# Kernel tuning notes

Hardware: AMD Instinct MI355X
Metric: run time of the kernel (lower is better)

The kernel has to match this reference:

```python
import jax, jax.numpy as jnp
import numpy as np

N = 50000   # nodes
E = 800000  # edges
R = 8       # relations
B = 4       # bases
NEG = 0.2   # leaky relu slope


def setup_inputs() -> dict:
    key = jax.random.key(0)
    ks = jax.random.split(key, 20)
    s = 0.1
    rn = lambda k, sh: jax.random.normal(k, sh, dtype=jnp.float32) * s
    return {
        "x": jax.random.normal(ks[0], (N, 64), dtype=jnp.float32),
        "edge_index": jax.random.randint(ks[1], (2, E), 0, N),
        "edge_type": jax.random.randint(ks[2], (E,), 0, R),
        # RGCN layer 1 (64 -> 64), basis decomposition
        "basis1": rn(ks[3], (B, 64, 64)), "comp1": rn(ks[4], (R, B)),
        "root1": rn(ks[5], (64, 64)), "brg1": jnp.zeros((64,), jnp.float32),
        # GAT layer 1 (64 -> 32, heads=4, concat -> 128)
        "wg1": rn(ks[6], (64, 128)), "asrc1": rn(ks[7], (4, 32)),
        "adst1": rn(ks[8], (4, 32)), "bg1": jnp.zeros((128,), jnp.float32),
        # RGCN layer 2 (128 -> 32)
        "basis2": rn(ks[9], (B, 128, 32)), "comp2": rn(ks[10], (R, B)),
        "root2": rn(ks[11], (128, 32)), "brg2": jnp.zeros((32,), jnp.float32),
        # GAT layer 2 (32 -> 16, heads=4, concat=False -> mean)
        "wg2": rn(ks[12], (32, 64)), "asrc2": rn(ks[13], (4, 16)),
        "adst2": rn(ks[14], (4, 16)), "bg2": jnp.zeros((16,), jnp.float32),
    }


def rgcn(x, src, dst, etype, basis, comp, root, bias):
    """PyG RGCNConv with basis decomposition, aggr='mean' per relation."""
    n, f = x.shape
    weight = jnp.einsum('rb,bio->rio', comp, basis)          # [R, in, out]
    seg = dst * R + etype                                    # per (node, relation) segment
    msg = x[src]                                             # [E, in] gather
    sums = jax.ops.segment_sum(msg, seg, num_segments=n * R).reshape(n, R, f)
    cnt = jax.ops.segment_sum(jnp.ones((src.shape[0],), x.dtype), seg,
                              num_segments=n * R).reshape(n, R, 1)
    mean = sums / jnp.maximum(cnt, 1.0)                      # [N, R, in]
    return jnp.einsum('nri,rio->no', mean, weight) + x @ root + bias


def gat(x, src, dst, w, a_src, a_dst, bias, heads, out_ch, concat):
    """PyG GATConv: add self loops, edge softmax over incoming edges."""
    n = x.shape[0]
    loop = jnp.arange(n)
    s2 = jnp.concatenate([src, loop])
    d2 = jnp.concatenate([dst, loop])
    h = (x @ w).reshape(n, heads, out_ch)                    # [N, H, C]
    al_src = (h * a_src).sum(-1)                             # [N, H]
    al_dst = (h * a_dst).sum(-1)                             # [N, H]
    e = jax.nn.leaky_relu(al_src[s2] + al_dst[d2], NEG)      # [E2, H]
    m = jax.ops.segment_max(e, d2, num_segments=n)           # stable softmax per dst
    e = jnp.exp(e - m[d2])
    z = jax.ops.segment_sum(e, d2, num_segments=n)
    alpha = e / z[d2]                                        # [E2, H]
    msg = h[s2] * alpha[:, :, None]                          # [E2, H, C]
    out = jax.ops.segment_sum(msg, d2, num_segments=n)       # [N, H, C]
    out = out.reshape(n, heads * out_ch) if concat else out.mean(axis=1)
    return out + bias


def reference(x, edge_index, edge_type,
              basis1, comp1, root1, brg1, wg1, asrc1, adst1, bg1,
              basis2, comp2, root2, brg2, wg2, asrc2, adst2, bg2):
    src, dst = edge_index[0], edge_index[1]
    # i=0: RGCN + relu (dropout p=0)
    x = jax.nn.relu(rgcn(x, src, dst, edge_type, basis1, comp1, root1, brg1))
    # i=1 == 2*pairs-1: GAT concat, NO activation
    x = gat(x, src, dst, wg1, asrc1, adst1, bg1, heads=4, out_ch=32, concat=True)
    # i=2: RGCN + relu
    x = jax.nn.relu(rgcn(x, src, dst, edge_type, basis2, comp2, root2, brg2))
    # i=3: GAT mean-heads + relu
    x = jax.nn.relu(gat(x, src, dst, wg2, asrc2, adst2, bg2, heads=4, out_ch=16, concat=False))
    return jnp.tanh(x)
```

## Files before the change

kernel.cpp:

```cpp
#include <hip/hip_runtime.h>
#include <math.h>

#define NN 50000
#define EE 800000
#define RR 8
#define SLOPE 0.2f
#define SEGS (NN * RR)
#define NTW ((NN + 63) / 64)
#define NBUK 98
#define SEGB 4096
#define EB4 ((EE + 4095) / 4096)

typedef __attribute__((ext_vector_type(8))) short bf16x8;
typedef __attribute__((ext_vector_type(4))) float f32x4;
typedef _Float16 f16;
typedef __attribute__((ext_vector_type(4))) _Float16 h4;
typedef __attribute__((ext_vector_type(8))) _Float16 h8;

__device__ __forceinline__ float leaky(float v) { return v >= 0.f ? v : SLOPE * v; }

__device__ __forceinline__ void fmacc(float4& a, const float4& v, float p) {
    a.x = fmaf(v.x, p, a.x);
    a.y = fmaf(v.y, p, a.y);
    a.z = fmaf(v.z, p, a.z);
    a.w = fmaf(v.w, p, a.w);
}

__device__ __forceinline__ void red4(float4& a, int m) {
    a.x += __shfl_xor(a.x, m);
    a.y += __shfl_xor(a.y, m);
    a.z += __shfl_xor(a.z, m);
    a.w += __shfl_xor(a.w, m);
}

__device__ __forceinline__ float4 h4tof4(h4 t) {
    return make_float4((float)t[0], (float)t[1], (float)t[2], (float)t[3]);
}

__device__ __forceinline__ h4 hmax4(h4 a, h4 b) {
    h4 r;
    r[0] = a[0] > b[0] ? a[0] : b[0];
    r[1] = a[1] > b[1] ? a[1] : b[1];
    r[2] = a[2] > b[2] ? a[2] : b[2];
    r[3] = a[3] > b[3] ? a[3] : b[3];
    return r;
}

__device__ __forceinline__ void split8(const float4& v0, const float4& v1,
                                       bf16x8& hi, bf16x8& lo) {
    float e[8] = {v0.x, v0.y, v0.z, v0.w, v1.x, v1.y, v1.z, v1.w};
    union { bf16x8 v; unsigned u[4]; } H, L;
#pragma unroll
    for (int j = 0; j < 4; j++) {
        unsigned b0 = __float_as_uint(e[2 * j]), b1 = __float_as_uint(e[2 * j + 1]);
        unsigned h0 = b0 & 0xFFFF0000u, h1 = b1 & 0xFFFF0000u;
        H.u[j] = (h0 >> 16) | h1;
        float l0 = e[2 * j] - __uint_as_float(h0);
        float l1 = e[2 * j + 1] - __uint_as_float(h1);
        L.u[j] = (__float_as_uint(l0) >> 16) | (__float_as_uint(l1) & 0xFFFF0000u);
    }
    hi = H.v;
    lo = L.v;
}

__global__ __launch_bounds__(256) void k_hist(const int* __restrict__ dst,
                                              int* __restrict__ buccnt) {
    __shared__ int h[NBUK];
    int tid = threadIdx.x;
    for (int i = tid; i < NBUK; i += 256) h[i] = 0;
    __syncthreads();
    int e0 = blockIdx.x * 4096;
    int cnt = EE - e0;
    if (cnt > 4096) cnt = 4096;
    for (int i = tid; i < cnt; i += 256) atomicAdd(&h[dst[e0 + i] >> 9], 1);
    __syncthreads();
    for (int i = tid; i < NBUK; i += 256)
        if (h[i]) atomicAdd(&buccnt[i], h[i]);
}

__global__ void k_scan98(const int* __restrict__ buccnt, int* __restrict__ bucbase,
                         int* __restrict__ cbcur) {
    __shared__ int sh[128];
    int t = threadIdx.x;
    int v = (t < NBUK) ? buccnt[t] : 0;
    sh[t] = v;
    __syncthreads();
    for (int off = 1; off < 128; off <<= 1) {
        int u = (t >= off) ? sh[t - off] : 0;
        __syncthreads();
        sh[t] += u;
        __syncthreads();
    }
    int excl = sh[t] - v;
    if (t <= NBUK) bucbase[t] = excl;
    if (t < NBUK) cbcur[t] = excl;
}

__global__ __launch_bounds__(256) void k_fillA(const int* __restrict__ src,
                                               const int* __restrict__ dst,
                                               const int* __restrict__ et,
                                               int* __restrict__ cbcur,
                                               int* __restrict__ recbuf) {
    __shared__ int hist[NBUK], lcur[NBUK], gres[NBUK];
    int tid = threadIdx.x;
    int e0 = blockIdx.x * 4096;
    int cnt = EE - e0;
    if (cnt > 4096) cnt = 4096;
    for (int i = tid; i < NBUK; i += 256) { hist[i] = 0; lcur[i] = 0; }
    __syncthreads();
    int myb[16], myrec[16];
#pragma unroll
    for (int j = 0; j < 16; j++) {
        int i = tid + j * 256;
        if (i < cnt) {
            int e = e0 + i;
            int d = dst[e];
            int b = d >> 9;
            myb[j] = b;
            myrec[j] = ((d & 511) << 19) | (src[e] << 3) | et[e];
            atomicAdd(&hist[b], 1);
        } else {
            myb[j] = -1;
            myrec[j] = 0;
        }
    }
    __syncthreads();
    if (tid < NBUK) gres[tid] = atomicAdd(&cbcur[tid], hist[tid]);
    __syncthreads();
#pragma unroll
    for (int j = 0; j < 16; j++) {
        if (myb[j] >= 0) {
            int p = atomicAdd(&lcur[myb[j]], 1);
            recbuf[gres[myb[j]] + p] = myrec[j];
        }
    }
}

__global__ __launch_bounds__(256) void k_fillB2(const int* __restrict__ bucbase,
                                                const int* __restrict__ recbuf,
                                                int* __restrict__ rp,
                                                int* __restrict__ srcs2) {
    __shared__ int cnt[SEGB];
    __shared__ int psc[256];
    int b = blockIdx.x;
    int segbase = b * SEGB;
    int nseg = SEGS - segbase;
    if (nseg > SEGB) nseg = SEGB;
    int base = bucbase[b];
    int cntE = bucbase[b + 1] - base;
    int tid = threadIdx.x;
    for (int s = tid; s < SEGB; s += 256) cnt[s] = 0;
    __syncthreads();
    for (int i = tid; i < cntE; i += 256) {
        int rec = recbuf[base + i];
        int segl = ((rec >> 19) << 3) | (rec & 7);
        atomicAdd(&cnt[segl], 1);
    }
    __syncthreads();
    int loc[16];
    int sbase = tid * 16;
    int run = 0;
#pragma unroll
    for (int j = 0; j < 16; j++) { loc[j] = cnt[sbase + j]; run += loc[j]; }
    psc[tid] = run;
    __syncthreads();
    for (int off = 1; off < 256; off <<= 1) {
        int u = (tid >= off) ? psc[tid - off] : 0;
        __syncthreads();
        psc[tid] += u;
        __syncthreads();
    }
    int excl = psc[tid] - run;
#pragma unroll
    for (int j = 0; j < 16; j++) {
        int s = sbase + j;
        int v = loc[j];
        cnt[s] = excl;
        if (s < nseg) rp[segbase + s] = base + excl;
        excl += v;
    }
    __syncthreads();
    for (int i = tid; i < cntE; i += 256) {
        int rec = recbuf[base + i];
        int segl = ((rec >> 19) << 3) | (rec & 7);
        int p = atomicAdd(&cnt[segl], 1);
        srcs2[base + p] = rec & 0x7FFFF;
    }
    if (b == NBUK - 1 && tid == 0) rp[SEGS] = EE;
}

__global__ void k_xh(const float* __restrict__ X, f16* __restrict__ xh) {
    int i = blockIdx.x * 256 + threadIdx.x;
    if (i >= NN * 8) return;
    float4 v0 = *(const float4*)(X + (size_t)i * 8);
    float4 v1 = *(const float4*)(X + (size_t)i * 8 + 4);
    h8 hv = {(f16)v0.x, (f16)v0.y, (f16)v0.z, (f16)v0.w,
             (f16)v1.x, (f16)v1.y, (f16)v1.z, (f16)v1.w};
    *(h8*)(xh + (size_t)i * 8) = hv;
}

__global__ void k_prep(const float* __restrict__ wg1, const float* __restrict__ wg2,
                       const float* __restrict__ root1, const float* __restrict__ root2,
                       const float* __restrict__ basis1, const float* __restrict__ basis2,
                       const float* __restrict__ comp2,
                       const float* __restrict__ asrc1, const float* __restrict__ adst1,
                       const float* __restrict__ asrc2, const float* __restrict__ adst2,
                       float* __restrict__ Wcat2e, float* __restrict__ wg1r,
                       float* __restrict__ Wstk, float* __restrict__ U1p,
                       float* __restrict__ U2p, float* __restrict__ Wb1) {
    int idx = blockIdx.x * 256 + threadIdx.x;
    if (idx < 16384) {
        int h = idx >> 12, kc = idx & 4095;
        int k = kc >> 6, c = kc & 63;
        wg1r[idx] = (c < 32) ? wg1[k * 128 + h * 32 + c] : 0.f;
    } else if (idx < 24576) {
        int j = idx - 16384;
        int row = j >> 6, c = j & 63;
        int h = row >> 5, k = row & 31;
        Wstk[j] = (c < 16) ? wg2[k * 64 + h * 16 + c] : 0.f;
    } else if (idx < 32768) {
        int j = idx - 24576;
        int k = j >> 6, c = j & 63;
        Wcat2e[k * 320 + c] = (c < 32) ? root2[k * 32 + c] : 0.f;
    } else if (idx < 36864) {
        int j0 = idx - 32768;
        int k = j0 >> 6, j = j0 & 63;
        float s = 0.f;
        if (j < 8) {
            int h = j & 3;
            const float* a = (j < 4) ? asrc1 : adst1;
            for (int c = 0; c < 32; c++) s += wg1[k * 128 + h * 32 + c] * a[h * 32 + c];
        }
        U1p[j0] = s;
    } else if (idx < 38912) {
        int j0 = idx - 36864;
        int k = j0 >> 6, j = j0 & 63;
        float s = 0.f;
        if (j < 8) {
            int h = j & 3;
            const float* a = (j < 4) ? asrc2 : adst2;
            for (int c = 0; c < 16; c++) s += wg2[k * 64 + h * 16 + c] * a[h * 16 + c];
        }
        U2p[j0] = s;
    } else if (idx < 55296) {
        Wb1[idx - 38912] = basis1[idx - 38912];
    } else if (idx < 59392) {
        Wb1[idx - 38912] = root1[idx - 55296];
    } else if (idx < 92160) {
        int j = idx - 59392;
        int i = j >> 8, rc = j & 255;
        int r = rc >> 5, o = rc & 31;
        float acc = 0.f;
#pragma unroll
        for (int b = 0; b < 4; b++) acc += comp2[r * 4 + b] * basis2[b * 4096 + i * 32 + o];
        Wcat2e[i * 320 + 64 + rc] = acc;
    }
}

__global__ void k_pack(const float* __restrict__ Wb1, const float* __restrict__ wg1r,
                       const float* __restrict__ Wcat, short* __restrict__ pWb1,
                       short* __restrict__ pwg1r, short* __restrict__ pWcat) {
    int u = blockIdx.x * 256 + threadIdx.x;
    int lane = u & 63, pair = u >> 6;
    if (pair >= 136) return;
    int m = lane & 15, g = lane >> 4;
    const float* src;
    int ldB, col, k0;
    short* dst;
    if (pair < 40) {
        int ct = pair / 10, kc = pair % 10;
        src = Wb1; ldB = 64; col = ct * 16 + m; k0 = kc * 32 + g * 8;
        dst = pWb1 + pair * 1024 + lane * 8;
    } else if (pair < 56) {
        int q = pair - 40;
        int h = q >> 2, lp = q & 3, ct = lp >> 1, kc = lp & 1;
        src = wg1r + h * 4096; ldB = 64; col = ct * 16 + m; k0 = kc * 32 + g * 8;
        dst = pwg1r + q * 1024 + lane * 8;
    } else {
        int q = pair - 56;
        int p = q >> 4, lp = q & 15, ct = lp >> 2, kc = lp & 3;
        src = Wcat; ldB = 320; col = p * 64 + ct * 16 + m; k0 = kc * 32 + g * 8;
        dst = pWcat + q * 1024 + lane * 8;
    }
    float e[8];
#pragma unroll
    for (int r = 0; r < 8; r++) e[r] = src[(size_t)(k0 + r) * ldB + col];
    union { bf16x8 v; unsigned u4[4]; } H, L;
#pragma unroll
    for (int j = 0; j < 4; j++) {
        unsigned b0 = __float_as_uint(e[2 * j]), b1 = __float_as_uint(e[2 * j + 1]);
        unsigned h0 = b0 & 0xFFFF0000u, h1 = b1 & 0xFFFF0000u;
        H.u4[j] = (h0 >> 16) | h1;
        float l0 = e[2 * j] - __uint_as_float(h0);
        float l1 = e[2 * j + 1] - __uint_as_float(h1);
        L.u4[j] = (__float_as_uint(l0) >> 16) | (__float_as_uint(l1) & 0xFFFF0000u);
    }
    *(bf16x8*)dst = H.v;
    *(bf16x8*)(dst + 512) = L.v;
}

template <int KTOT, int NCOL, int ACT = 0, int OUTH = 0, int AH = 0>
__global__ __launch_bounds__(256) void k_mfma(const float* __restrict__ X, int ldX, int xmb,
                                              const short* __restrict__ Bpk, int bmb,
                                              float* __restrict__ Y, int ldY, size_t ymb,
                                              const float* __restrict__ bias, int biasmb) {
    constexpr int NKC = KTOT / 32;
    constexpr int NCT = NCOL / 16;
    const int tid = threadIdx.x;
    const int wid = tid >> 6, lane = tid & 63;
    const int m = lane & 15, g = lane >> 4;
    const int mb = blockIdx.y;
    const int rowbase = blockIdx.x * 64 + wid * 16;
    if (rowbase >= NN) return;
    const float* Xm = X + (size_t)mb * xmb + (size_t)(rowbase + m) * ldX;
    const f16* Xmh = (const f16*)X + (size_t)mb * xmb + (size_t)(rowbase + m) * ldX;
    const short* Bm = Bpk + (size_t)mb * bmb;

    f32x4 acc[NCT];
#pragma unroll
    for (int c = 0; c < NCT; c++) acc[c] = (f32x4){0.f, 0.f, 0.f, 0.f};

#pragma unroll
    for (int kc = 0; kc < NKC; kc++) {
        float4 v0, v1;
        if (AH) {
            h8 hv = *(const h8*)(Xmh + kc * 32 + g * 8);
            v0 = make_float4((float)hv[0], (float)hv[1], (float)hv[2], (float)hv[3]);
            v1 = make_float4((float)hv[4], (float)hv[5], (float)hv[6], (float)hv[7]);
        } else {
            v0 = *(const float4*)(Xm + kc * 32 + g * 8);
            v1 = *(const float4*)(Xm + kc * 32 + g * 8 + 4);
        }
        bf16x8 ah, al;
        split8(v0, v1, ah, al);
#pragma unroll
        for (int ct = 0; ct < NCT; ct++) {
            const short* bp = Bm + (size_t)(ct * NKC + kc) * 1024 + lane * 8;
            bf16x8 bh = *(const bf16x8*)bp;
            bf16x8 bl = *(const bf16x8*)(bp + 512);
            acc[ct] = __builtin_amdgcn_mfma_f32_16x16x32_bf16(ah, bh, acc[ct], 0, 0, 0);
            acc[ct] = __builtin_amdgcn_mfma_f32_16x16x32_bf16(al, bh, acc[ct], 0, 0, 0);
            acc[ct] = __builtin_amdgcn_mfma_f32_16x16x32_bf16(ah, bl, acc[ct], 0, 0, 0);
        }
    }

#pragma unroll
    for (int ct = 0; ct < NCT; ct++) {
        int col = ct * 16 + m;
        float bv = bias ? bias[mb * biasmb + col] : 0.f;
#pragma unroll
        for (int i = 0; i < 4; i++) {
            float o = acc[ct][i] + bv;
            if (ACT == 2) o = fmaxf(o, 0.f);
            if (OUTH) {
                f16* Yh = (f16*)Y;
                Yh[(size_t)mb * ymb + (size_t)(rowbase + g * 4 + i) * ldY + col] = (f16)o;
            } else {
                Y[(size_t)mb * ymb + (size_t)(rowbase + g * 4 + i) * ldY + col] = o;
            }
        }
    }
}

__global__ __launch_bounds__(256) void k_mfmaL3(const f16* __restrict__ Xh,
                                                const short* __restrict__ Bpk,
                                                float* __restrict__ x3,
                                                f16* __restrict__ ybuf3h) {
    const int tid = threadIdx.x;
    const int wid = tid >> 6, lane = tid & 63;
    const int m = lane & 15, g = lane >> 4;
    const int y = blockIdx.y;
    const int rowbase = blockIdx.x * 64 + wid * 16;
    if (rowbase >= NN) return;
    const f16* Xm = Xh + (size_t)(rowbase + m) * 128;

    f32x4 acc[6];
#pragma unroll
    for (int j = 0; j < 6; j++) acc[j] = (f32x4){0.f, 0.f, 0.f, 0.f};

#pragma unroll
    for (int kc = 0; kc < 4; kc++) {
        h8 hv = *(const h8*)(Xm + kc * 32 + g * 8);
        float4 v0 = make_float4((float)hv[0], (float)hv[1], (float)hv[2], (float)hv[3]);
        float4 v1 = make_float4((float)hv[4], (float)hv[5], (float)hv[6], (float)hv[7]);
        bf16x8 ah, al;
        split8(v0, v1, ah, al);
#pragma unroll
        for (int j = 0; j < 6; j++) {
            int bct = (y == 0) ? ((j < 2) ? j : j + 2) : (8 + (y - 1) * 6 + j);
            const short* bp = Bpk + (size_t)(bct * 4 + kc) * 1024 + lane * 8;
            bf16x8 bh = *(const bf16x8*)bp;
            bf16x8 bl = *(const bf16x8*)(bp + 512);
            acc[j] = __builtin_amdgcn_mfma_f32_16x16x32_bf16(ah, bh, acc[j], 0, 0, 0);
            acc[j] = __builtin_amdgcn_mfma_f32_16x16x32_bf16(al, bh, acc[j], 0, 0, 0);
            acc[j] = __builtin_amdgcn_mfma_f32_16x16x32_bf16(ah, bl, acc[j], 0, 0, 0);
        }
    }
#pragma unroll
    for (int j = 0; j < 6; j++) {
        int bct = (y == 0) ? ((j < 2) ? j : j + 2) : (8 + (y - 1) * 6 + j);
        if (bct < 2) {
            int col = bct * 16 + m;
#pragma unroll
            for (int r = 0; r < 4; r++) {
                int n = rowbase + g * 4 + r;
                x3[(size_t)n * 32 + col] = acc[j][r];
            }
        } else {
            int gcol = bct * 16 + m - 64;
            int p = gcol >> 6, cc = gcol & 63;
            f16* Yp = ybuf3h + (size_t)p * NN * 64;
#pragma unroll
            for (int r = 0; r < 4; r++) {
                int n = rowbase + g * 4 + r;
                Yp[(size_t)n * 64 + cc] = (f16)acc[j][r];
            }
        }
    }
}

__global__ __launch_bounds__(256) void k_gagg1(const int* __restrict__ rp,
                                               const int* __restrict__ srcs2,
                                               const float* __restrict__ comp,
                                               const f16* __restrict__ Xh,
                                               f16* __restrict__ Uh) {
    __shared__ float4 sh_w[4][8];
    int wid = threadIdx.x >> 6, lane = threadIdx.x & 63;
    int n = blockIdx.x * 4 + wid;
    int rpv = (lane <= 8) ? rp[n * RR + lane] : 0;
    int nxt = __shfl(rpv, (lane + 1) & 63);
    if (lane < 8) {
        float inv = 1.f / (float)((nxt - rpv) > 0 ? (nxt - rpv) : 1);
        float4 c = *(const float4*)(comp + lane * 4);
        sh_w[wid][lane] = make_float4(c.x * inv, c.y * inv, c.z * inv, c.w * inv);
    }
    int q = lane & 15;
    int beg = rp[n * RR], end = rp[n * RR + RR];
    float4 a0 = make_float4(0.f, 0.f, 0.f, 0.f);
    float4 a1 = a0, a2 = a0, a3 = a0;
    int k = beg + (lane >> 4);
    for (; k + 4 < end; k += 8) {
        int key0 = srcs2[k], key1 = srcs2[k + 4];
        float4 w0 = sh_w[wid][key0 & 7], w1 = sh_w[wid][key1 & 7];
        float4 v0 = h4tof4(*(const h4*)(Xh + (size_t)(key0 >> 3) * 64 + q * 4));
        float4 v1 = h4tof4(*(const h4*)(Xh + (size_t)(key1 >> 3) * 64 + q * 4));
        fmacc(a0, v0, w0.x);
        fmacc(a1, v0, w0.y);
        fmacc(a2, v0, w0.z);
        fmacc(a3, v0, w0.w);
        fmacc(a0, v1, w1.x);
        fmacc(a1, v1, w1.y);
        fmacc(a2, v1, w1.z);
        fmacc(a3, v1, w1.w);
    }
    if (k < end) {
        int key0 = srcs2[k];
        float4 w0 = sh_w[wid][key0 & 7];
        float4 v0 = h4tof4(*(const h4*)(Xh + (size_t)(key0 >> 3) * 64 + q * 4));
        fmacc(a0, v0, w0.x);
        fmacc(a1, v0, w0.y);
        fmacc(a2, v0, w0.z);
        fmacc(a3, v0, w0.w);
    }
    red4(a0, 16); red4(a0, 32);
    red4(a1, 16); red4(a1, 32);
    red4(a2, 16); red4(a2, 32);
    red4(a3, 16); red4(a3, 32);
    if (lane < 16) {
        f16* un = Uh + (size_t)n * 320;
        h4 o0 = {(f16)a0.x, (f16)a0.y, (f16)a0.z, (f16)a0.w};
        h4 o1 = {(f16)a1.x, (f16)a1.y, (f16)a1.z, (f16)a1.w};
        h4 o2 = {(f16)a2.x, (f16)a2.y, (f16)a2.z, (f16)a2.w};
        h4 o3 = {(f16)a3.x, (f16)a3.y, (f16)a3.z, (f16)a3.w};
        *(h4*)(un + 0 * 64 + q * 4) = o0;
        *(h4*)(un + 1 * 64 + q * 4) = o1;
        *(h4*)(un + 2 * 64 + q * 4) = o2;
        *(h4*)(un + 3 * 64 + q * 4) = o3;
        *(h4*)(un + 256 + q * 4) = *(const h4*)(Xh + (size_t)n * 64 + q * 4);
    }
}

__global__ __launch_bounds__(256) void k_alds1(const f16* __restrict__ X1h,
                                               const float* __restrict__ U1p,
                                               f16* __restrict__ aldsEh) {
    __shared__ float sUT[8 * 68];
    int tid = threadIdx.x;
    for (int i = tid; i < 512; i += 256) {
        int j = i >> 6, c = i & 63;
        sUT[j * 68 + c] = U1p[c * 64 + j];
    }
    __syncthreads();
    int lane = tid & 63, wid = tid >> 6;
    int n = blockIdx.x * 32 + wid * 8 + (lane >> 3);
    int q = lane & 7;
    float x[8];
    if (n < NN) {
        h8 hv = *(const h8*)(X1h + (size_t)n * 64 + q * 8);
#pragma unroll
        for (int c = 0; c < 8; c++) x[c] = (float)hv[c];
    } else {
#pragma unroll
        for (int c = 0; c < 8; c++) x[c] = 0.f;
    }
    float al[8];
#pragma unroll
    for (int j = 0; j < 8; j++) {
        const float* u = &sUT[j * 68 + q * 8];
        float s = 0.f;
#pragma unroll
        for (int c = 0; c < 8; c++) s += x[c] * u[c];
        al[j] = s;
    }
#pragma unroll
    for (int m = 1; m < 8; m <<= 1)
#pragma unroll
        for (int j = 0; j < 8; j++) al[j] += __shfl_xor(al[j], m);
    if (n < NN) {
        float av = al[q];
        int pos = (q < 4) ? q : q + 4;
        aldsEh[(size_t)n * 16 + pos] = (f16)__expf(av);
        aldsEh[(size_t)n * 16 + pos + 4] = (f16)__expf(SLOPE * av);
    }
}

__global__ __launch_bounds__(256) void k_final(const f16* __restrict__ Xm,
                                               const float* __restrict__ Wstk,
                                               const float* __restrict__ bg2,
                                               float* __restrict__ out) {
    __shared__ float sWT[16 * 132];
    int tid = threadIdx.x;
    for (int i = tid; i < 2048; i += 256) {
        int c = i >> 7, k = i & 127;
        sWT[c * 132 + k] = Wstk[k * 64 + c];
    }
    __syncthreads();
    int lane = tid & 63, wid = tid >> 6;
    int n = blockIdx.x * 32 + wid * 8 + (lane >> 3);
    int q = lane & 7;
    float x[16];
    if (n < NN) {
#pragma unroll
        for (int t = 0; t < 4; t++) {
            float4 v = h4tof4(*(const h4*)(Xm + (size_t)n * 128 + t * 32 + q * 4));
            x[t * 4 + 0] = v.x; x[t * 4 + 1] = v.y; x[t * 4 + 2] = v.z; x[t * 4 + 3] = v.w;
        }
    } else {
#pragma unroll
        for (int k = 0; k < 16; k++) x[k] = 0.f;
    }
    float al[16];
#pragma unroll
    for (int c = 0; c < 16; c++) {
        float s = 0.f;
#pragma unroll
        for (int t = 0; t < 4; t++) {
            const float* w = &sWT[c * 132 + t * 32 + q * 4];
            s += x[t * 4 + 0] * w[0] + x[t * 4 + 1] * w[1] + x[t * 4 + 2] * w[2] +
                 x[t * 4 + 3] * w[3];
        }
        al[c] = s;
    }
#pragma unroll
    for (int m = 1; m < 8; m <<= 1)
#pragma unroll
        for (int c = 0; c < 16; c++) al[c] += __shfl_xor(al[c], m);
    if (n < NN && q < 4) {
        float4 bv = *(const float4*)(bg2 + q * 4);
        float4 v;
        v.x = tanhf(fmaxf(0.25f * al[q * 4 + 0] + bv.x, 0.f));
        v.y = tanhf(fmaxf(0.25f * al[q * 4 + 1] + bv.y, 0.f));
        v.z = tanhf(fmaxf(0.25f * al[q * 4 + 2] + bv.z, 0.f));
        v.w = tanhf(fmaxf(0.25f * al[q * 4 + 3] + bv.w, 0.f));
        *(float4*)(out + (size_t)n * 16 + q * 4) = v;
    }
}

__global__ __launch_bounds__(256) void k_agg2(const int* __restrict__ rp,
                                              const int* __restrict__ srcs2,
                                              const f16* __restrict__ y,
                                              const float* __restrict__ bias,
                                              const float* __restrict__ U2p,
                                              const float* __restrict__ x3prev,
                                              f16* __restrict__ x3h,
                                              f16* __restrict__ aldsEh) {
    __shared__ float sh_inv[4][8];
    int wid = threadIdx.x >> 6, lane = threadIdx.x & 63;
    int n = blockIdx.x * 4 + wid;
    int rpv = (lane <= 8) ? rp[n * RR + lane] : 0;
    int nxt = __shfl(rpv, (lane + 1) & 63);
    if (lane < 8) sh_inv[wid][lane] = 1.f / (float)((nxt - rpv) > 0 ? (nxt - rpv) : 1);
    int q = lane & 7;
    int beg = rp[n * RR], end = rp[n * RR + RR];
    float4 acc = make_float4(0.f, 0.f, 0.f, 0.f);
    int k = beg + (lane >> 3);
    for (; k + 8 < end; k += 16) {
        int key0 = srcs2[k], key1 = srcs2[k + 8];
        int s0 = key0 >> 3, s1 = key1 >> 3;
        int g0 = key0 & 7, g1 = key1 & 7;
        float e0 = sh_inv[wid][g0], e1 = sh_inv[wid][g1];
        float4 v0 = h4tof4(*(const h4*)(y + ((size_t)(g0 >> 1) * NN + s0) * 64 + (g0 & 1) * 32 + q * 4));
        float4 v1 = h4tof4(*(const h4*)(y + ((size_t)(g1 >> 1) * NN + s1) * 64 + (g1 & 1) * 32 + q * 4));
        fmacc(acc, v0, e0);
        fmacc(acc, v1, e1);
    }
    if (k < end) {
        int key0 = srcs2[k];
        int s0 = key0 >> 3;
        int g0 = key0 & 7;
        float4 v0 = h4tof4(*(const h4*)(y + ((size_t)(g0 >> 1) * NN + s0) * 64 + (g0 & 1) * 32 + q * 4));
        fmacc(acc, v0, sh_inv[wid][g0]);
    }
    red4(acc, 8);
    red4(acc, 16);
    red4(acc, 32);
    if (lane < 8) {
        float4 prev = *(const float4*)(x3prev + (size_t)n * 32 + q * 4);
        float4 b = *(const float4*)(bias + q * 4);
        float4 v;
        v.x = fmaxf(prev.x + acc.x + b.x, 0.f);
        v.y = fmaxf(prev.y + acc.y + b.y, 0.f);
        v.z = fmaxf(prev.z + acc.z + b.z, 0.f);
        v.w = fmaxf(prev.w + acc.w + b.w, 0.f);
        h4 hv = {(f16)v.x, (f16)v.y, (f16)v.z, (f16)v.w};
        *(h4*)(x3h + (size_t)n * 32 + q * 4) = hv;
        float al[8];
#pragma unroll
        for (int j = 0; j < 8; j++) {
            al[j] = fmaf(v.x, U2p[(q * 4 + 0) * 64 + j],
                    fmaf(v.y, U2p[(q * 4 + 1) * 64 + j],
                    fmaf(v.z, U2p[(q * 4 + 2) * 64 + j],
                         v.w * U2p[(q * 4 + 3) * 64 + j])));
        }
#pragma unroll
        for (int m = 1; m < 8; m <<= 1) {
#pragma unroll
            for (int j = 0; j < 8; j++) al[j] += __shfl_xor(al[j], m);
        }
        float av = al[q];
        int pos = (q < 4) ? q : q + 4;
        aldsEh[(size_t)n * 16 + pos] = (f16)__expf(av);
        aldsEh[(size_t)n * 16 + pos + 4] = (f16)__expf(SLOPE * av);
    }
}

template <int F, int LDX = F>
__global__ __launch_bounds__(256) void k_gatx(const int* __restrict__ rp,
                                              const int* __restrict__ srcs2,
                                              const f16* __restrict__ aldsEh,
                                              const f16* __restrict__ X,
                                              f16* __restrict__ msg) {
    constexpr int G = F / 4;
    constexpr int NG = 64 / G;
    int wid = threadIdx.x >> 6, lane = threadIdx.x & 63;
    int n = blockIdx.x * 4 + wid;
    if (n >= NN) return;
    int g = lane / G, q = lane % G;
    h4 EdH = *(const h4*)(aldsEh + (size_t)n * 16 + 8);
    h4 Ed2H = *(const h4*)(aldsEh + (size_t)n * 16 + 12);
    float4 acc0 = make_float4(0.f, 0.f, 0.f, 0.f);
    float4 acc1 = acc0, acc2 = acc0, acc3 = acc0;
    float4 z = make_float4(0.f, 0.f, 0.f, 0.f);
    if (g == 0) {
        h4 es = *(const h4*)(aldsEh + (size_t)n * 16);
        h4 es2 = *(const h4*)(aldsEh + (size_t)n * 16 + 4);
        float4 xv = h4tof4(*(const h4*)(X + (size_t)n * LDX + q * 4));
        h4 pH = hmax4(es * EdH, es2 * Ed2H);
        float p0 = (float)pH[0], p1 = (float)pH[1], p2 = (float)pH[2], p3 = (float)pH[3];
        z = make_float4(p0, p1, p2, p3);
        fmacc(acc0, xv, p0);
        fmacc(acc1, xv, p1);
        fmacc(acc2, xv, p2);
        fmacc(acc3, xv, p3);
    }
    int beg = rp[n * RR], end = rp[n * RR + RR];
    int k = beg + g;
    for (; k + NG < end; k += 2 * NG) {
        int s0 = srcs2[k] >> 3, s1 = srcs2[k + NG] >> 3;
        h8 e0 = *(const h8*)(aldsEh + (size_t)s0 * 16);
        h8 e1 = *(const h8*)(aldsEh + (size_t)s1 * 16);
        float4 x0 = h4tof4(*(const h4*)(X + (size_t)s0 * LDX + q * 4));
        float4 x1v = h4tof4(*(const h4*)(X + (size_t)s1 * LDX + q * 4));
        h4 e0lo = {e0[0], e0[1], e0[2], e0[3]};
        h4 e0hi = {e0[4], e0[5], e0[6], e0[7]};
        h4 e1lo = {e1[0], e1[1], e1[2], e1[3]};
        h4 e1hi = {e1[4], e1[5], e1[6], e1[7]};
        h4 p0H = hmax4(e0lo * EdH, e0hi * Ed2H);
        h4 p1H = hmax4(e1lo * EdH, e1hi * Ed2H);
        float p00 = (float)p0H[0], p01 = (float)p0H[1], p02 = (float)p0H[2], p03 = (float)p0H[3];
        float p10 = (float)p1H[0], p11 = (float)p1H[1], p12 = (float)p1H[2], p13 = (float)p1H[3];
        z.x += p00 + p10;
        z.y += p01 + p11;
        z.z += p02 + p12;
        z.w += p03 + p13;
        fmacc(acc0, x0, p00);
        fmacc(acc1, x0, p01);
        fmacc(acc2, x0, p02);
        fmacc(acc3, x0, p03);
        fmacc(acc0, x1v, p10);
        fmacc(acc1, x1v, p11);
        fmacc(acc2, x1v, p12);
        fmacc(acc3, x1v, p13);
    }
    if (k < end) {
        int s0 = srcs2[k] >> 3;
        h8 e0 = *(const h8*)(aldsEh + (size_t)s0 * 16);
        float4 x0 = h4tof4(*(const h4*)(X + (size_t)s0 * LDX + q * 4));
        h4 e0lo = {e0[0], e0[1], e0[2], e0[3]};
        h4 e0hi = {e0[4], e0[5], e0[6], e0[7]};
        h4 p0H = hmax4(e0lo * EdH, e0hi * Ed2H);
        float p00 = (float)p0H[0], p01 = (float)p0H[1], p02 = (float)p0H[2], p03 = (float)p0H[3];
        z.x += p00;
        z.y += p01;
        z.z += p02;
        z.w += p03;
        fmacc(acc0, x0, p00);
        fmacc(acc1, x0, p01);
        fmacc(acc2, x0, p02);
        fmacc(acc3, x0, p03);
    }
#pragma unroll
    for (int m = G; m < 64; m <<= 1) {
        red4(acc0, m);
        red4(acc1, m);
        red4(acc2, m);
        red4(acc3, m);
        red4(z, m);
    }
    if (g == 0) {
        float4 iz = make_float4(1.f / z.x, 1.f / z.y, 1.f / z.z, 1.f / z.w);
        f16* mp = msg + (size_t)n * 4 * F + q * 4;
        h4 o0 = {(f16)(acc0.x * iz.x), (f16)(acc0.y * iz.x), (f16)(acc0.z * iz.x), (f16)(acc0.w * iz.x)};
        h4 o1 = {(f16)(acc1.x * iz.y), (f16)(acc1.y * iz.y), (f16)(acc1.z * iz.y), (f16)(acc1.w * iz.y)};
        h4 o2 = {(f16)(acc2.x * iz.z), (f16)(acc2.y * iz.z), (f16)(acc2.z * iz.z), (f16)(acc2.w * iz.z)};
        h4 o3 = {(f16)(acc3.x * iz.w), (f16)(acc3.y * iz.w), (f16)(acc3.z * iz.w), (f16)(acc3.w * iz.w)};
        *(h4*)(mp + 0 * F) = o0;
        *(h4*)(mp + 1 * F) = o1;
        *(h4*)(mp + 2 * F) = o2;
        *(h4*)(mp + 3 * F) = o3;
    }
}

extern "C" void kernel_launch(void* const* d_in, const int* in_sizes, int n_in,
                              void* d_out, int out_size, void* d_ws, size_t ws_size,
                              hipStream_t stream) {
    const float* x      = (const float*)d_in[0];
    const int*   ei     = (const int*)d_in[1];
    const int*   et     = (const int*)d_in[2];
    const float* basis1 = (const float*)d_in[3];
    const float* comp1  = (const float*)d_in[4];
    const float* root1  = (const float*)d_in[5];
    const float* brg1   = (const float*)d_in[6];
    const float* wg1    = (const float*)d_in[7];
    const float* asrc1  = (const float*)d_in[8];
    const float* adst1  = (const float*)d_in[9];
    const float* bg1    = (const float*)d_in[10];
    const float* basis2 = (const float*)d_in[11];
    const float* comp2  = (const float*)d_in[12];
    const float* root2  = (const float*)d_in[13];
    const float* brg2   = (const float*)d_in[14];
    const float* wg2    = (const float*)d_in[15];
    const float* asrc2  = (const float*)d_in[16];
    const float* adst2  = (const float*)d_in[17];
    const float* bg2    = (const float*)d_in[18];
    const int* src = ei;
    const int* dst = ei + EE;
    float* out = (float*)d_out;

    int* wsi = (int*)d_ws;
    size_t ioff = 0;
    auto ialloc = [&](size_t n) { int* p = wsi + ioff; ioff += (n + 3) & ~(size_t)3; return p; };
    int* rp   = ialloc(SEGS + 1);
    int* srcs2 = ialloc(EE);
    int* recbuf = ialloc(EE);
    int* cbcur = ialloc(128);
    int* buccnt = ialloc(128);
    int* bucbase = ialloc(128);
    float* wsf = (float*)(wsi + ioff);
    size_t total_f = (ws_size - ioff * sizeof(int)) / sizeof(float);
    size_t P_f = (size_t)NN * 320;
    size_t need_f = P_f + (size_t)NN * 128
                  + 40960 + 20480 + 16384 + 8192 + 4096 + 2048
                  + (size_t)NN * 8
                  + 20480 + 8192 + 40960
                  + (size_t)NN * 32 + (size_t)NN * 16 + (size_t)NN * 32 + 64;
    if (total_f < need_f) return;
    size_t foff = 0;
    auto falloc = [&](size_t n) { float* p = wsf + foff; foff += (n + 3) & ~(size_t)3; return p; };
    float* P      = falloc(P_f);
    float* x2     = falloc((size_t)NN * 128);
    float* Wcat2e = falloc(40960);
    float* Wb1    = falloc(20480);
    float* wg1r   = falloc(16384);
    float* Wstk   = falloc(8192);
    float* U1p    = falloc(4096);
    float* U2p    = falloc(2048);
    f16* aldsEh   = (f16*)falloc((size_t)NN * 8);
    short* Wb1pk  = (short*)falloc(20480);
    short* wg1rpk = (short*)falloc(8192);
    short* Wcatpk = (short*)falloc(40960);
    f16* x1h      = (f16*)falloc((size_t)NN * 32);
    f16* x3h      = (f16*)falloc((size_t)NN * 16);
    f16* xh       = (f16*)falloc((size_t)NN * 32);
    f16* Uh = (f16*)P;
    f16* x2h = (f16*)x2;
    f16* msg1h  = (f16*)P;
    float* x3   = P;
    f16* ybuf3h = (f16*)(P + (size_t)NN * 64);
    f16* msg2h  = (f16*)(P + (size_t)NN * 64);

    const int NB4 = (NN + 3) / 4;
    const int NB32 = (NN + 31) / 32;

    hipMemsetAsync(buccnt, 0, 128 * sizeof(int), stream);
    k_hist<<<EB4, 256, 0, stream>>>(dst, buccnt);
    k_scan98<<<1, 128, 0, stream>>>(buccnt, bucbase, cbcur);
    k_fillA<<<EB4, 256, 0, stream>>>(src, dst, et, cbcur, recbuf);
    k_fillB2<<<NBUK, 256, 0, stream>>>(bucbase, recbuf, rp, srcs2);
    k_xh<<<(NN * 8 + 255) / 256, 256, 0, stream>>>(x, xh);
    k_prep<<<(92160 + 255) / 256, 256, 0, stream>>>(
        wg1, wg2, root1, root2, basis1, basis2, comp2, asrc1, adst1, asrc2, adst2,
        Wcat2e, wg1r, Wstk, U1p, U2p, Wb1);
    k_pack<<<34, 256, 0, stream>>>(Wb1, wg1r, Wcat2e, Wb1pk, wg1rpk, Wcatpk);

    k_gagg1<<<NB4, 256, 0, stream>>>(rp, srcs2, comp1, xh, Uh);
    k_mfma<320, 64, 2, 1, 1><<<dim3(NTW, 1), 256, 0, stream>>>((const float*)Uh, 320, 0,
                                                               Wb1pk, 0,
                                                               (float*)x1h, 64, 0, brg1, 0);

    k_alds1<<<NB32, 256, 0, stream>>>(x1h, U1p, aldsEh);
    k_gatx<64, 64><<<NB4, 256, 0, stream>>>(rp, srcs2, aldsEh, x1h, msg1h);
    k_mfma<64, 32, 0, 1, 1><<<dim3(NTW, 4), 256, 0, stream>>>((const float*)msg1h, 256, 64,
                                                              wg1rpk, 4096,
                                                              (float*)x2h, 128, 32, bg1, 32);

    k_mfmaL3<<<dim3(NTW, 3), 256, 0, stream>>>(x2h, Wcatpk, x3, ybuf3h);
    k_agg2<<<NB4, 256, 0, stream>>>(rp, srcs2, ybuf3h, brg2, U2p, x3, x3h, aldsEh);

    k_gatx<32, 32><<<NB4, 256, 0, stream>>>(rp, srcs2, aldsEh, x3h, msg2h);
    k_final<<<NB32, 256, 0, stream>>>(msg2h, Wstk, bg2, out);
}
```

Baseline: 386.9 us.

## Switch to fp16 MFMA and fp16 accumulation; fuse histogram with x conversion

Replaces the 3-pass bf16 hi/lo split MFMA with a 2-pass fp16 scheme (fp16 activations times hi/lo fp16 weights). The gather-aggregation kernels (gagg1, gatx) now accumulate in packed fp16 instead of fp32. Separately, the x-to-fp16 conversion kernel is merged into the edge histogram kernel to save a launch. This cuts MFMA count, conversion ALU work and register pressure, at the risk of fp16 overflow or precision loss in long accumulations over high-degree nodes.

```diff
diff --git a/kernel.cpp b/kernel.cpp
--- a/kernel.cpp
+++ b/kernel.cpp
@@ -10,14 +10,12 @@
 #define NBUK 98
 #define SEGB 4096
 #define EB4 ((EE + 4095) / 4096)
-
-typedef __attribute__((ext_vector_type(8))) short bf16x8;
+#define XB ((NN * 8 + 255) / 256)
+
 typedef __attribute__((ext_vector_type(4))) float f32x4;
 typedef _Float16 f16;
 typedef __attribute__((ext_vector_type(4))) _Float16 h4;
 typedef __attribute__((ext_vector_type(8))) _Float16 h8;
-
-__device__ __forceinline__ float leaky(float v) { return v >= 0.f ? v : SLOPE * v; }
 
 __device__ __forceinline__ void fmacc(float4& a, const float4& v, float p) {
     a.x = fmaf(v.x, p, a.x);
@@ -46,36 +44,34 @@
     return r;
 }
 
-__device__ __forceinline__ void split8(const float4& v0, const float4& v1,
-                                       bf16x8& hi, bf16x8& lo) {
-    float e[8] = {v0.x, v0.y, v0.z, v0.w, v1.x, v1.y, v1.z, v1.w};
-    union { bf16x8 v; unsigned u[4]; } H, L;
-#pragma unroll
-    for (int j = 0; j < 4; j++) {
-        unsigned b0 = __float_as_uint(e[2 * j]), b1 = __float_as_uint(e[2 * j + 1]);
-        unsigned h0 = b0 & 0xFFFF0000u, h1 = b1 & 0xFFFF0000u;
-        H.u[j] = (h0 >> 16) | h1;
-        float l0 = e[2 * j] - __uint_as_float(h0);
-        float l1 = e[2 * j + 1] - __uint_as_float(h1);
-        L.u[j] = (__float_as_uint(l0) >> 16) | (__float_as_uint(l1) & 0xFFFF0000u);
-    }
-    hi = H.v;
-    lo = L.v;
-}
-
-__global__ __launch_bounds__(256) void k_hist(const int* __restrict__ dst,
-                                              int* __restrict__ buccnt) {
+__device__ __forceinline__ h4 hsplat(f16 s) { return (h4){s, s, s, s}; }
+
+__global__ __launch_bounds__(256) void k_histxh(const int* __restrict__ dst,
+                                                int* __restrict__ buccnt,
+                                                const float* __restrict__ X,
+                                                f16* __restrict__ xh) {
     __shared__ int h[NBUK];
+    int b = blockIdx.x;
     int tid = threadIdx.x;
-    for (int i = tid; i < NBUK; i += 256) h[i] = 0;
-    __syncthreads();
-    int e0 = blockIdx.x * 4096;
-    int cnt = EE - e0;
-    if (cnt > 4096) cnt = 4096;
-    for (int i = tid; i < cnt; i += 256) atomicAdd(&h[dst[e0 + i] >> 9], 1);
-    __syncthreads();
-    for (int i = tid; i < NBUK; i += 256)
-        if (h[i]) atomicAdd(&buccnt[i], h[i]);
+    if (b < EB4) {
+        for (int i = tid; i < NBUK; i += 256) h[i] = 0;
+        __syncthreads();
+        int e0 = b * 4096;
+        int cnt = EE - e0;
+        if (cnt > 4096) cnt = 4096;
+        for (int i = tid; i < cnt; i += 256) atomicAdd(&h[dst[e0 + i] >> 9], 1);
+        __syncthreads();
+        for (int i = tid; i < NBUK; i += 256)
+            if (h[i]) atomicAdd(&buccnt[i], h[i]);
+    } else {
+        int i = (b - EB4) * 256 + tid;
+        if (i >= NN * 8) return;
+        float4 v0 = *(const float4*)(X + (size_t)i * 8);
+        float4 v1 = *(const float4*)(X + (size_t)i * 8 + 4);
+        h8 hv = {(f16)v0.x, (f16)v0.y, (f16)v0.z, (f16)v0.w,
+                 (f16)v1.x, (f16)v1.y, (f16)v1.z, (f16)v1.w};
+        *(h8*)(xh + (size_t)i * 8) = hv;
+    }
 }
 
 __global__ void k_scan98(const int* __restrict__ buccnt, int* __restrict__ bucbase,
@@ -187,16 +183,6 @@
         srcs2[base + p] = rec & 0x7FFFF;
     }
     if (b == NBUK - 1 && tid == 0) rp[SEGS] = EE;
-}
-
-__global__ void k_xh(const float* __restrict__ X, f16* __restrict__ xh) {
-    int i = blockIdx.x * 256 + threadIdx.x;
-    if (i >= NN * 8) return;
-    float4 v0 = *(const float4*)(X + (size_t)i * 8);
-    float4 v1 = *(const float4*)(X + (size_t)i * 8 + 4);
-    h8 hv = {(f16)v0.x, (f16)v0.y, (f16)v0.z, (f16)v0.w,
-             (f16)v1.x, (f16)v1.y, (f16)v1.z, (f16)v1.w};
-    *(h8*)(xh + (size_t)i * 8) = hv;
 }
 
 __global__ void k_prep(const float* __restrict__ wg1, const float* __restrict__ wg2,
@@ -282,25 +268,20 @@
         src = Wcat; ldB = 320; col = p * 64 + ct * 16 + m; k0 = kc * 32 + g * 8;
         dst = pWcat + q * 1024 + lane * 8;
     }
-    float e[8];
-#pragma unroll
-    for (int r = 0; r < 8; r++) e[r] = src[(size_t)(k0 + r) * ldB + col];
-    union { bf16x8 v; unsigned u4[4]; } H, L;
-#pragma unroll
-    for (int j = 0; j < 4; j++) {
-        unsigned b0 = __float_as_uint(e[2 * j]), b1 = __float_as_uint(e[2 * j + 1]);
-        unsigned h0 = b0 & 0xFFFF0000u, h1 = b1 & 0xFFFF0000u;
-        H.u4[j] = (h0 >> 16) | h1;
-        float l0 = e[2 * j] - __uint_as_float(h0);
-        float l1 = e[2 * j + 1] - __uint_as_float(h1);
-        L.u4[j] = (__float_as_uint(l0) >> 16) | (__float_as_uint(l1) & 0xFFFF0000u);
-    }
-    *(bf16x8*)dst = H.v;
-    *(bf16x8*)(dst + 512) = L.v;
-}
-
-template <int KTOT, int NCOL, int ACT = 0, int OUTH = 0, int AH = 0>
-__global__ __launch_bounds__(256) void k_mfma(const float* __restrict__ X, int ldX, int xmb,
+    h8 H, L;
+#pragma unroll
+    for (int r = 0; r < 8; r++) {
+        float e = src[(size_t)(k0 + r) * ldB + col];
+        f16 hi = (f16)e;
+        H[r] = hi;
+        L[r] = (f16)(e - (float)hi);
+    }
+    *(h8*)dst = H;
+    *(h8*)(dst + 512) = L;
+}
+
+template <int KTOT, int NCOL, int ACT = 0, int OUTH = 0>
+__global__ __launch_bounds__(256) void k_mfma(const f16* __restrict__ X, int ldX, int xmb,
                                               const short* __restrict__ Bpk, int bmb,
                                               float* __restrict__ Y, int ldY, size_t ymb,
                                               const float* __restrict__ bias, int biasmb) {
@@ -312,8 +293,7 @@
     const int mb = blockIdx.y;
     const int rowbase = blockIdx.x * 64 + wid * 16;
     if (rowbase >= NN) return;
-    const float* Xm = X + (size_t)mb * xmb + (size_t)(rowbase + m) * ldX;
-    const f16* Xmh = (const f16*)X + (size_t)mb * xmb + (size_t)(rowbase + m) * ldX;
+    const f16* Xm = X + (size_t)mb * xmb + (size_t)(rowbase + m) * ldX;
     const short* Bm = Bpk + (size_t)mb * bmb;
 
     f32x4 acc[NCT];
@@ -322,25 +302,14 @@
 
 #pragma unroll
     for (int kc = 0; kc < NKC; kc++) {
-        float4 v0, v1;
-        if (AH) {
-            h8 hv = *(const h8*)(Xmh + kc * 32 + g * 8);
-            v0 = make_float4((float)hv[0], (float)hv[1], (float)hv[2], (float)hv[3]);
-            v1 = make_float4((float)hv[4], (float)hv[5], (float)hv[6], (float)hv[7]);
-        } else {
-            v0 = *(const float4*)(Xm + kc * 32 + g * 8);
-            v1 = *(const float4*)(Xm + kc * 32 + g * 8 + 4);
-        }
-        bf16x8 ah, al;
-        split8(v0, v1, ah, al);
+        h8 av = *(const h8*)(Xm + kc * 32 + g * 8);
 #pragma unroll
         for (int ct = 0; ct < NCT; ct++) {
             const short* bp = Bm + (size_t)(ct * NKC + kc) * 1024 + lane * 8;
-            bf16x8 bh = *(const bf16x8*)bp;
-            bf16x8 bl = *(const bf16x8*)(bp + 512);
-            acc[ct] = __builtin_amdgcn_mfma_f32_16x16x32_bf16(ah, bh, acc[ct], 0, 0, 0);
-            acc[ct] = __builtin_amdgcn_mfma_f32_16x16x32_bf16(al, bh, acc[ct], 0, 0, 0);
-            acc[ct] = __builtin_amdgcn_mfma_f32_16x16x32_bf16(ah, bl, acc[ct], 0, 0, 0);
+            h8 bh = *(const h8*)bp;
+            h8 bl = *(const h8*)(bp + 512);
+            acc[ct] = __builtin_amdgcn_mfma_f32_16x16x32_f16(av, bh, acc[ct], 0, 0, 0);
+            acc[ct] = __builtin_amdgcn_mfma_f32_16x16x32_f16(av, bl, acc[ct], 0, 0, 0);
         }
     }
 
@@ -380,20 +349,15 @@
 
 #pragma unroll
     for (int kc = 0; kc < 4; kc++) {
-        h8 hv = *(const h8*)(Xm + kc * 32 + g * 8);
-        float4 v0 = make_float4((float)hv[0], (float)hv[1], (float)hv[2], (float)hv[3]);
-        float4 v1 = make_float4((float)hv[4], (float)hv[5], (float)hv[6], (float)hv[7]);
-        bf16x8 ah, al;
-        split8(v0, v1, ah, al);
+        h8 av = *(const h8*)(Xm + kc * 32 + g * 8);
 #pragma unroll
         for (int j = 0; j < 6; j++) {
             int bct = (y == 0) ? ((j < 2) ? j : j + 2) : (8 + (y - 1) * 6 + j);
             const short* bp = Bpk + (size_t)(bct * 4 + kc) * 1024 + lane * 8;
-            bf16x8 bh = *(const bf16x8*)bp;
-            bf16x8 bl = *(const bf16x8*)(bp + 512);
-            acc[j] = __builtin_amdgcn_mfma_f32_16x16x32_bf16(ah, bh, acc[j], 0, 0, 0);
-            acc[j] = __builtin_amdgcn_mfma_f32_16x16x32_bf16(al, bh, acc[j], 0, 0, 0);
-            acc[j] = __builtin_amdgcn_mfma_f32_16x16x32_bf16(ah, bl, acc[j], 0, 0, 0);
+            h8 bh = *(const h8*)bp;
+            h8 bl = *(const h8*)(bp + 512);
+            acc[j] = __builtin_amdgcn_mfma_f32_16x16x32_f16(av, bh, acc[j], 0, 0, 0);
+            acc[j] = __builtin_amdgcn_mfma_f32_16x16x32_f16(av, bl, acc[j], 0, 0, 0);
         }
     }
 #pragma unroll
@@ -424,7 +388,7 @@
                                                const float* __restrict__ comp,
                                                const f16* __restrict__ Xh,
                                                f16* __restrict__ Uh) {
-    __shared__ float4 sh_w[4][8];
+    __shared__ h4 sh_w[4][8];
     int wid = threadIdx.x >> 6, lane = threadIdx.x & 63;
     int n = blockIdx.x * 4 + wid;
     int rpv = (lane <= 8) ? rp[n * RR + lane] : 0;
@@ -432,46 +396,48 @@
     if (lane < 8) {
         float inv = 1.f / (float)((nxt - rpv) > 0 ? (nxt - rpv) : 1);
         float4 c = *(const float4*)(comp + lane * 4);
-        sh_w[wid][lane] = make_float4(c.x * inv, c.y * inv, c.z * inv, c.w * inv);
+        sh_w[wid][lane] = (h4){(f16)(c.x * inv), (f16)(c.y * inv),
+                               (f16)(c.z * inv), (f16)(c.w * inv)};
     }
     int q = lane & 15;
     int beg = rp[n * RR], end = rp[n * RR + RR];
-    float4 a0 = make_float4(0.f, 0.f, 0.f, 0.f);
-    float4 a1 = a0, a2 = a0, a3 = a0;
+    h4 hz = {(f16)0.f, (f16)0.f, (f16)0.f, (f16)0.f};
+    h4 a0 = hz, a1 = hz, a2 = hz, a3 = hz;
     int k = beg + (lane >> 4);
     for (; k + 4 < end; k += 8) {
         int key0 = srcs2[k], key1 = srcs2[k + 4];
-        float4 w0 = sh_w[wid][key0 & 7], w1 = sh_w[wid][key1 & 7];
-        float4 v0 = h4tof4(*(const h4*)(Xh + (size_t)(key0 >> 3) * 64 + q * 4));
-        float4 v1 = h4tof4(*(const h4*)(Xh + (size_t)(key1 >> 3) * 64 + q * 4));
-        fmacc(a0, v0, w0.x);
-        fmacc(a1, v0, w0.y);
-        fmacc(a2, v0, w0.z);
-        fmacc(a3, v0, w0.w);
-        fmacc(a0, v1, w1.x);
-        fmacc(a1, v1, w1.y);
-        fmacc(a2, v1, w1.z);
-        fmacc(a3, v1, w1.w);
+        h4 w0 = sh_w[wid][key0 & 7], w1 = sh_w[wid][key1 & 7];
+        h4 v0 = *(const h4*)(Xh + (size_t)(key0 >> 3) * 64 + q * 4);
+        h4 v1 = *(const h4*)(Xh + (size_t)(key1 >> 3) * 64 + q * 4);
+        a0 += hsplat(w0[0]) * v0;
+        a1 += hsplat(w0[1]) * v0;
+        a2 += hsplat(w0[2]) * v0;
+        a3 += hsplat(w0[3]) * v0;
+        a0 += hsplat(w1[0]) * v1;
+        a1 += hsplat(w1[1]) * v1;
+        a2 += hsplat(w1[2]) * v1;
+        a3 += hsplat(w1[3]) * v1;
     }
     if (k < end) {
         int key0 = srcs2[k];
-        float4 w0 = sh_w[wid][key0 & 7];
-        float4 v0 = h4tof4(*(const h4*)(Xh + (size_t)(key0 >> 3) * 64 + q * 4));
-        fmacc(a0, v0, w0.x);
-        fmacc(a1, v0, w0.y);
-        fmacc(a2, v0, w0.z);
-        fmacc(a3, v0, w0.w);
-    }
-    red4(a0, 16); red4(a0, 32);
-    red4(a1, 16); red4(a1, 32);
-    red4(a2, 16); red4(a2, 32);
-    red4(a3, 16); red4(a3, 32);
+        h4 w0 = sh_w[wid][key0 & 7];
+        h4 v0 = *(const h4*)(Xh + (size_t)(key0 >> 3) * 64 + q * 4);
+        a0 += hsplat(w0[0]) * v0;
+        a1 += hsplat(w0[1]) * v0;
+        a2 += hsplat(w0[2]) * v0;
+        a3 += hsplat(w0[3]) * v0;
+    }
+    float4 A0 = h4tof4(a0), A1 = h4tof4(a1), A2 = h4tof4(a2), A3 = h4tof4(a3);
+    red4(A0, 16); red4(A0, 32);
+    red4(A1, 16); red4(A1, 32);
+    red4(A2, 16); red4(A2, 32);
+    red4(A3, 16); red4(A3, 32);
     if (lane < 16) {
         f16* un = Uh + (size_t)n * 320;
-        h4 o0 = {(f16)a0.x, (f16)a0.y, (f16)a0.z, (f16)a0.w};
-        h4 o1 = {(f16)a1.x, (f16)a1.y, (f16)a1.z, (f16)a1.w};
-        h4 o2 = {(f16)a2.x, (f16)a2.y, (f16)a2.z, (f16)a2.w};
-        h4 o3 = {(f16)a3.x, (f16)a3.y, (f16)a3.z, (f16)a3.w};
+        h4 o0 = {(f16)A0.x, (f16)A0.y, (f16)A0.z, (f16)A0.w};
+        h4 o1 = {(f16)A1.x, (f16)A1.y, (f16)A1.z, (f16)A1.w};
+        h4 o2 = {(f16)A2.x, (f16)A2.y, (f16)A2.z, (f16)A2.w};
+        h4 o3 = {(f16)A3.x, (f16)A3.y, (f16)A3.z, (f16)A3.w};
         *(h4*)(un + 0 * 64 + q * 4) = o0;
         *(h4*)(un + 1 * 64 + q * 4) = o1;
         *(h4*)(un + 2 * 64 + q * 4) = o2;
@@ -657,20 +623,18 @@
     int g = lane / G, q = lane % G;
     h4 EdH = *(const h4*)(aldsEh + (size_t)n * 16 + 8);
     h4 Ed2H = *(const h4*)(aldsEh + (size_t)n * 16 + 12);
-    float4 acc0 = make_float4(0.f, 0.f, 0.f, 0.f);
-    float4 acc1 = acc0, acc2 = acc0, acc3 = acc0;
-    float4 z = make_float4(0.f, 0.f, 0.f, 0.f);
+    h4 hz = {(f16)0.f, (f16)0.f, (f16)0.f, (f16)0.f};
+    h4 acc0 = hz, acc1 = hz, acc2 = hz, acc3 = hz, zH = hz;
     if (g == 0) {
         h4 es = *(const h4*)(aldsEh + (size_t)n * 16);
         h4 es2 = *(const h4*)(aldsEh + (size_t)n * 16 + 4);
-        float4 xv = h4tof4(*(const h4*)(X + (size_t)n * LDX + q * 4));
+        h4 xv = *(const h4*)(X + (size_t)n * LDX + q * 4);
         h4 pH = hmax4(es * EdH, es2 * Ed2H);
-        float p0 = (float)pH[0], p1 = (float)pH[1], p2 = (float)pH[2], p3 = (float)pH[3];
-        z = make_float4(p0, p1, p2, p3);
-        fmacc(acc0, xv, p0);
-        fmacc(acc1, xv, p1);
-        fmacc(acc2, xv, p2);
-        fmacc(acc3, xv, p3);
+        zH += pH;
+        acc0 += hsplat(pH[0]) * xv;
+        acc1 += hsplat(pH[1]) * xv;
+        acc2 += hsplat(pH[2]) * xv;
+        acc3 += hsplat(pH[3]) * xv;
     }
     int beg = rp[n * RR], end = rp[n * RR + RR];
     int k = beg + g;
@@ -678,61 +642,54 @@
         int s0 = srcs2[k] >> 3, s1 = srcs2[k + NG] >> 3;
         h8 e0 = *(const h8*)(aldsEh + (size_t)s0 * 16);
         h8 e1 = *(const h8*)(aldsEh + (size_t)s1 * 16);
-        float4 x0 = h4tof4(*(const h4*)(X + (size_t)s0 * LDX + q * 4));
-        float4 x1v = h4tof4(*(const h4*)(X + (size_t)s1 * LDX + q * 4));
+        h4 x0 = *(const h4*)(X + (size_t)s0 * LDX + q * 4);
+        h4 x1v = *(const h4*)(X + (size_t)s1 * LDX + q * 4);
         h4 e0lo = {e0[0], e0[1], e0[2], e0[3]};
         h4 e0hi = {e0[4], e0[5], e0[6], e0[7]};
         h4 e1lo = {e1[0], e1[1], e1[2], e1[3]};
         h4 e1hi = {e1[4], e1[5], e1[6], e1[7]};
         h4 p0H = hmax4(e0lo * EdH, e0hi * Ed2H);
         h4 p1H = hmax4(e1lo * EdH, e1hi * Ed2H);
-        float p00 = (float)p0H[0], p01 = (float)p0H[1], p02 = (float)p0H[2], p03 = (float)p0H[3];
-        float p10 = (float)p1H[0], p11 = (float)p1H[1], p12 = (float)p1H[2], p13 = (float)p1H[3];
-        z.x += p00 + p10;
-        z.y += p01 + p11;
-        z.z += p02 + p12;
-        z.w += p03 + p13;
-        fmacc(acc0, x0, p00);
-        fmacc(acc1, x0, p01);
-        fmacc(acc2, x0, p02);
-        fmacc(acc3, x0, p03);
-        fmacc(acc0, x1v, p10);
-        fmacc(acc1, x1v, p11);
-        fmacc(acc2, x1v, p12);
-        fmacc(acc3, x1v, p13);
+        zH += p0H + p1H;
+        acc0 += hsplat(p0H[0]) * x0;
+        acc1 += hsplat(p0H[1]) * x0;
+        acc2 += hsplat(p0H[2]) * x0;
+        acc3 += hsplat(p0H[3]) * x0;
+        acc0 += hsplat(p1H[0]) * x1v;
+        acc1 += hsplat(p1H[1]) * x1v;
+        acc2 += hsplat(p1H[2]) * x1v;
+        acc3 += hsplat(p1H[3]) * x1v;
     }
     if (k < end) {
         int s0 = srcs2[k] >> 3;
         h8 e0 = *(const h8*)(aldsEh + (size_t)s0 * 16);
-        float4 x0 = h4tof4(*(const h4*)(X + (size_t)s0 * LDX + q * 4));
+        h4 x0 = *(const h4*)(X + (size_t)s0 * LDX + q * 4);
         h4 e0lo = {e0[0], e0[1], e0[2], e0[3]};
         h4 e0hi = {e0[4], e0[5], e0[6], e0[7]};
         h4 p0H = hmax4(e0lo * EdH, e0hi * Ed2H);
-        float p00 = (float)p0H[0], p01 = (float)p0H[1], p02 = (float)p0H[2], p03 = (float)p0H[3];
-        z.x += p00;
-        z.y += p01;
-        z.z += p02;
-        z.w += p03;
-        fmacc(acc0, x0, p00);
-        fmacc(acc1, x0, p01);
-        fmacc(acc2, x0, p02);
-        fmacc(acc3, x0, p03);
-    }
+        zH += p0H;
+        acc0 += hsplat(p0H[0]) * x0;
+        acc1 += hsplat(p0H[1]) * x0;
+        acc2 += hsplat(p0H[2]) * x0;
+        acc3 += hsplat(p0H[3]) * x0;
+    }
+    float4 A0 = h4tof4(acc0), A1 = h4tof4(acc1), A2 = h4tof4(acc2), A3 = h4tof4(acc3);
+    float4 z = h4tof4(zH);
 #pragma unroll
     for (int m = G; m < 64; m <<= 1) {
-        red4(acc0, m);
-        red4(acc1, m);
-        red4(acc2, m);
-        red4(acc3, m);
+        red4(A0, m);
+        red4(A1, m);
+        red4(A2, m);
+        red4(A3, m);
         red4(z, m);
     }
     if (g == 0) {
         float4 iz = make_float4(1.f / z.x, 1.f / z.y, 1.f / z.z, 1.f / z.w);
         f16* mp = msg + (size_t)n * 4 * F + q * 4;
-        h4 o0 = {(f16)(acc0.x * iz.x), (f16)(acc0.y * iz.x), (f16)(acc0.z * iz.x), (f16)(acc0.w * iz.x)};
-        h4 o1 = {(f16)(acc1.x * iz.y), (f16)(acc1.y * iz.y), (f16)(acc1.z * iz.y), (f16)(acc1.w * iz.y)};
-        h4 o2 = {(f16)(acc2.x * iz.z), (f16)(acc2.y * iz.z), (f16)(acc2.z * iz.z), (f16)(acc2.w * iz.z)};
-        h4 o3 = {(f16)(acc3.x * iz.w), (f16)(acc3.y * iz.w), (f16)(acc3.z * iz.w), (f16)(acc3.w * iz.w)};
+        h4 o0 = {(f16)(A0.x * iz.x), (f16)(A0.y * iz.x), (f16)(A0.z * iz.x), (f16)(A0.w * iz.x)};
+        h4 o1 = {(f16)(A1.x * iz.y), (f16)(A1.y * iz.y), (f16)(A1.z * iz.y), (f16)(A1.w * iz.y)};
+        h4 o2 = {(f16)(A2.x * iz.z), (f16)(A2.y * iz.z), (f16)(A2.z * iz.z), (f16)(A2.w * iz.z)};
+        h4 o3 = {(f16)(A3.x * iz.w), (f16)(A3.y * iz.w), (f16)(A3.z * iz.w), (f16)(A3.w * iz.w)};
         *(h4*)(mp + 0 * F) = o0;
         *(h4*)(mp + 1 * F) = o1;
         *(h4*)(mp + 2 * F) = o2;
@@ -812,26 +769,23 @@
     const int NB32 = (NN + 31) / 32;
 
     hipMemsetAsync(buccnt, 0, 128 * sizeof(int), stream);
-    k_hist<<<EB4, 256, 0, stream>>>(dst, buccnt);
+    k_histxh<<<EB4 + XB, 256, 0, stream>>>(dst, buccnt, x, xh);
     k_scan98<<<1, 128, 0, stream>>>(buccnt, bucbase, cbcur);
     k_fillA<<<EB4, 256, 0, stream>>>(src, dst, et, cbcur, recbuf);
     k_fillB2<<<NBUK, 256, 0, stream>>>(bucbase, recbuf, rp, srcs2);
-    k_xh<<<(NN * 8 + 255) / 256, 256, 0, stream>>>(x, xh);
     k_prep<<<(92160 + 255) / 256, 256, 0, stream>>>(
         wg1, wg2, root1, root2, basis1, basis2, comp2, asrc1, adst1, asrc2, adst2,
         Wcat2e, wg1r, Wstk, U1p, U2p, Wb1);
     k_pack<<<34, 256, 0, stream>>>(Wb1, wg1r, Wcat2e, Wb1pk, wg1rpk, Wcatpk);
 
     k_gagg1<<<NB4, 256, 0, stream>>>(rp, srcs2, comp1, xh, Uh);
-    k_mfma<320, 64, 2, 1, 1><<<dim3(NTW, 1), 256, 0, stream>>>((const float*)Uh, 320, 0,
-                                                               Wb1pk, 0,
-                                                               (float*)x1h, 64, 0, brg1, 0);
+    k_mfma<320, 64, 2, 1><<<dim3(NTW, 1), 256, 0, stream>>>(Uh, 320, 0, Wb1pk, 0,
+                                                            (float*)x1h, 64, 0, brg1, 0);
 
     k_alds1<<<NB32, 256, 0, stream>>>(x1h, U1p, aldsEh);
     k_gatx<64, 64><<<NB4, 256, 0, stream>>>(rp, srcs2, aldsEh, x1h, msg1h);
-    k_mfma<64, 32, 0, 1, 1><<<dim3(NTW, 4), 256, 0, stream>>>((const float*)msg1h, 256, 64,
-                                                              wg1rpk, 4096,
-                                                              (float*)x2h, 128, 32, bg1, 32);
+    k_mfma<64, 32, 0, 1><<<dim3(NTW, 4), 256, 0, stream>>>(msg1h, 256, 64, wg1rpk, 4096,
+                                                           (float*)x2h, 128, 32, bg1, 32);
 
     k_mfmaL3<<<dim3(NTW, 3), 256, 0, stream>>>(x2h, Wcatpk, x3, ybuf3h);
     k_agg2<<<NB4, 256, 0, stream>>>(rp, srcs2, ybuf3h, brg2, U2p, x3, x3h, aldsEh);
```

Measured after the change: 381.3 us, median of 2. No clear change (-1.4%).
